# Kernel tuning notes

Measured on AMD Instinct MI355X. Metric: run time of the kernel, lower is better.

Reference implementation:

```python
import jax, jax.numpy as jnp
import numpy as np

B, T, D = 16, 2048, 512
DB, K, TOPK, WIN = 128, 7, 16, 64
GATE_CAP = 0.5
STRAND_CAP = 0.5
_PHI = 1.618033988749895
_PSI = -0.6180339887498949


def _ln(x, w, b):
    mu = jnp.mean(x, -1, keepdims=True)
    var = jnp.var(x, -1, keepdims=True)
    return (x - mu) * jax.lax.rsqrt(var + 1e-5) * w + b


def setup_inputs() -> dict:
    key = jax.random.key(0)
    ks = jax.random.split(key, 20)
    def nrm(i, shape, scale=1.0):
        return jax.random.normal(ks[i], shape, dtype=jnp.float32) * jnp.float32(scale)
    return {
        'X_write': nrm(0, (B, T, D)),
        'X_read': nrm(1, (B, T, D)),
        'slots': nrm(2, (B, K, DB)),
        'W0': nrm(3, (D, D), D ** -0.5),
        'ln_write_w': jnp.ones((D,), jnp.float32),
        'ln_write_b': jnp.zeros((D,), jnp.float32),
        'W_V': nrm(4, (D, DB), D ** -0.5),
        'W_K_slot': nrm(5, (DB, DB), DB ** -0.5),
        'slot_key_bias': nrm(6, (K, DB), 2.0),
        'W_gate_w': nrm(7, (2 * DB, DB), (2 * DB) ** -0.5),
        'W_gate_b': jnp.full((DB,), -2.0, jnp.float32),
        'ln_strand_w': jnp.ones((DB,), jnp.float32),
        'ln_strand_b': jnp.zeros((DB,), jnp.float32),
        'Ws_Q': nrm(8, (DB, DB), DB ** -0.5),
        'Ws_K': nrm(9, (DB, DB), DB ** -0.5),
        'Ws_V': nrm(10, (DB, DB), DB ** -0.5),
        'lambda_strand': nrm(11, (DB,), 0.5),
        'W_Q_read': nrm(12, (D, DB), D ** -0.5),
        'W_K_read': nrm(13, (DB, DB), DB ** -0.5),
        'W_V_read': nrm(14, (DB, D), DB ** -0.5),
        'render_coeffs': nrm(15, (K, 3, D), 0.2),
        'slot_temps': jnp.ones((K,), jnp.float32),
    }


def _forward(X_write, X_read, slots, W0, ln_write_w, ln_write_b, W_V, W_K_slot,
             slot_key_bias, W_gate_w, W_gate_b, ln_strand_w, ln_strand_b,
             Ws_Q, Ws_K, Ws_V, lambda_strand, W_Q_read, W_K_read, W_V_read,
             render_coeffs, slot_temps):
    scale = jnp.float32(DB ** -0.5)
    W0_sg = jax.lax.stop_gradient(W0)
    X_n = _ln(X_write, ln_write_w, ln_write_b)

    # ---- windowed salience + topk pair selection (no-grad in original) ----
    X_nsg = jax.lax.stop_gradient(X_n)
    X_W0 = X_nsg @ W0_sg.T                      # [B,T,D]
    NEG = jnp.float32(-1e30)
    sal = []
    for o in range(1, WIN + 1):                 # offset j = i - o, fixed small loop
        s = jnp.sum(X_nsg[:, o:, :] * X_W0[:, :-o, :], axis=-1)  # [B, T-o]
        sal.append(jnp.pad(s, ((0, 0), (o, 0)), constant_values=NEG))
    sal = jnp.stack(sal, axis=-1).reshape(B, T * WIN)
    _, flat_idx = jax.lax.top_k(sal, TOPK)      # [B, TOPK]
    i_idx = flat_idx // WIN
    j_idx = i_idx - (flat_idx % WIN + 1)

    # ---- gather pairs, salience-weighted relation vector ----
    x_newer = jnp.take_along_axis(X_n, i_idx[:, :, None], axis=1)   # [B,TOPK,D]
    x_older = jnp.take_along_axis(X_n, j_idx[:, :, None], axis=1)
    pair_sal = jnp.sum(x_newer * (x_older @ W0_sg.T), axis=-1)      # [B,TOPK]
    alpha = jax.nn.softmax(pair_sal, axis=-1)
    rel = (x_newer - x_older) @ W_V                                 # [B,TOPK,DB]
    R_t = jnp.einsum('bk,bkd->bd', alpha, rel)                      # [B,DB]

    # ---- gated slot write ----
    slot_keys = slots @ W_K_slot + slot_key_bias                    # [B,K,DB]
    compat = jnp.einsum('bkd,bd->bk', slot_keys, R_t) * scale * jax.nn.softplus(slot_temps)
    sw = jax.nn.softmax(compat, axis=-1)
    weighted_R = sw[:, :, None] * R_t[:, None, :]                   # [B,K,DB]
    g = jax.nn.sigmoid(jnp.concatenate([slots, weighted_R], -1) @ W_gate_w + W_gate_b)
    slots_upd = (1.0 - g) * slots + g * weighted_R

    # ---- K x K strand mixer ----
    Bn = _ln(slots_upd, ln_strand_w, ln_strand_b)
    sa = jax.nn.softmax(jnp.einsum('bqd,bkd->bqk', Bn @ Ws_Q, Bn @ Ws_K) * scale, axis=-1)
    ctx = sa @ (Bn @ Ws_V)
    slots_next = slots_upd + ctx * jnp.clip(jnp.tanh(lambda_strand), -STRAND_CAP, STRAND_CAP)

    # ---- aux losses ----
    L_persist = jnp.mean((slots_next - slots) ** 2)
    nrm = jnp.maximum(jnp.linalg.norm(slots_next, axis=-1, keepdims=True), 1e-12)
    Bnorm = slots_next / nrm
    cos = jnp.einsum('bkd,bjd->bkj', Bnorm, Bnorm)
    off = ~jnp.eye(K, dtype=bool)
    L_div = jnp.mean((cos ** 2)[:, off])

    # ---- directional gated read attention ----
    q_r = X_read @ W_Q_read                                         # [B,T,DB]
    k_r = slots_next @ W_K_read                                     # [B,K,DB]
    v_r = slots_next @ W_V_read                                     # [B,K,D]
    scores = jnp.einsum('btd,bkd->btk', q_r, k_r) * scale
    q_mean = jnp.mean(X_read, axis=1)                               # [B,D]
    w0q = q_mean @ W0_sg.T
    denom = jnp.float32(_PHI - _PSI)
    phi_q = (w0q - _PSI * q_mean) / denom
    psi_q = (_PHI * q_mean - w0q) / denom
    phi_mag = jnp.linalg.norm(phi_q, axis=-1, keepdims=True)
    psi_mag = jnp.linalg.norm(psi_q, axis=-1, keepdims=True)
    total = phi_mag + psi_mag + 1e-6
    basis = jnp.concatenate([jnp.ones_like(phi_mag), phi_mag / total, psi_mag / total], -1)  # [B,3]
    gate = jnp.clip(jnp.tanh(jnp.einsum('bi,kid->bkd', basis, render_coeffs)), -GATE_CAP, GATE_CAP)
    z = jnp.einsum('btk,bkd->btd', jax.nn.softmax(scores, axis=-1), v_r * gate)
    return z, slots_next, L_persist, L_div


def reference(X_write, X_read, slots, W0, ln_write_w, ln_write_b, W_V, W_K_slot,
              slot_key_bias, W_gate_w, W_gate_b, ln_strand_w, ln_strand_b,
              Ws_Q, Ws_K, Ws_V, lambda_strand, W_Q_read, W_K_read, W_V_read,
              render_coeffs, slot_temps):
    return _forward(X_write, X_read, slots, W0, ln_write_w, ln_write_b, W_V, W_K_slot,
                    slot_key_bias, W_gate_w, W_gate_b, ln_strand_w, ln_strand_b,
                    Ws_Q, Ws_K, Ws_V, lambda_strand, W_Q_read, W_K_read, W_V_read,
                    render_coeffs, slot_temps)
```

## Files before the change

### kernel.cpp

```cpp
#include <hip/hip_runtime.h>
#include <math.h>

#define B_ 16
#define T_ 2048
#define D_ 512
#define DB_ 128
#define K_ 7
#define TOPK_ 16
#define WIN_ 64

static constexpr float SCALE_ = 0.08838834764831845f;
static constexpr float PHI_ = 1.618033988749895f;
static constexpr float PSI_ = -0.6180339887498949f;
static constexpr float INV_DENOM_ = 0.4472135954999579f;
static constexpr float NEGV = -1e30f;
static constexpr float NEGINF = -3.402823466e38f;
#define IMAXI 0x7FFFFFFF

typedef __attribute__((ext_vector_type(8))) __bf16 bf16x8;
typedef __attribute__((ext_vector_type(8))) unsigned short u16x8;
typedef __attribute__((ext_vector_type(4))) float f32x4;

__device__ inline float softplusf(float x){
    return fmaxf(x, 0.f) + log1pf(expf(-fabsf(x)));
// ... 208 lines not shown
        rAh = *(const uint4*)(XhB + (size_t)(i0 + ar)*512 + kk + ac*8);
        rAl = *(const uint4*)(XlB + (size_t)(i0 + ar)*512 + kk + ac*8);
        #pragma unroll
        for (int cc = 0; cc < 2; cc++) {
            int c = 2*bhh + cc;
            if (jrow >= 0) {
                const float* src = CfB + (size_t)jrow*512 + kk + c*8;
                rB0[cc] = *(const float4*)src;
                rB1[cc] = *(const float4*)(src + 4);
            } else {
                rB0[cc] = make_float4(0.f,0.f,0.f,0.f);
                rB1[cc] = make_float4(0.f,0.f,0.f,0.f);
            }
        }
    };
    auto WRITE = [&](){
        *(uint4*)&sAh[ar*32 + aslot*8] = rAh;
        *(uint4*)&sAl[ar*32 + aslot*8] = rAl;
        #pragma unroll
        for (int cc = 0; cc < 2; cc++) {
            int c = 2*bhh + cc;
            int slot = (c + (brow >> 1)) & 3;
            uint4 hv, lv;
            float4 v0 = rB0[cc], v1 = rB1[cc];
            unsigned int h01 = pkbf(v0.x, v0.y), h23 = pkbf(v0.z, v0.w);
            unsigned int h45 = pkbf(v1.x, v1.y), h67 = pkbf(v1.z, v1.w);
            float r0 = v0.x - __uint_as_float(h01 << 16);
            float r1 = v0.y - __uint_as_float(h01 & 0xFFFF0000u);
            float r2 = v0.z - __uint_as_float(h23 << 16);
            float r3 = v0.w - __uint_as_float(h23 & 0xFFFF0000u);
            float r4 = v1.x - __uint_as_float(h45 << 16);
            float r5 = v1.y - __uint_as_float(h45 & 0xFFFF0000u);
            float r6 = v1.z - __uint_as_float(h67 << 16);
            float r7 = v1.w - __uint_as_float(h67 & 0xFFFF0000u);
            hv.x = h01; hv.y = h23; hv.z = h45; hv.w = h67;
            lv.x = pkbf(r0, r1); lv.y = pkbf(r2, r3); lv.z = pkbf(r4, r5); lv.w = pkbf(r6, r7);
            *(uint4*)&sBh[brow*32 + slot*8] = hv;
            *(uint4*)&sBl[brow*32 + slot*8] = lv;
        }
    };

    LOAD(0);
    for (int t = 0; t < 16; t++) {
        WRITE();
        __syncthreads();
        int kkn = (t+1)*32;
        bf16x8 ahf[4], alf[4], bhf[2], blf[2];
        #pragma unroll
        for (int m = 0; m < 4; m++) {
            int r = (m*16 + fr)*32 + kc2;
            ahf[m] = ld_bf8(&sAh[r]);
            alf[m] = ld_bf8(&sAl[r]);
        }
        #pragma unroll
        for (int n = 0; n < 2; n++) {
            int r = (wcw*32 + n*16 + fr)*32 + kc2;
            bhf[n] = ld_bf8(&sBh[r]);
            blf[n] = ld_bf8(&sBl[r]);
        }
        if (t < 15) LOAD(kkn);
        #pragma unroll
        for (int m = 0; m < 4; m++)
            #pragma unroll
            for (int n = 0; n < 2; n++) {
                acc[m][n] = __builtin_amdgcn_mfma_f32_16x16x32_bf16(ahf[m], bhf[n], acc[m][n], 0, 0, 0);
                acc[m][n] = __builtin_amdgcn_mfma_f32_16x16x32_bf16(ahf[m], blf[n], acc[m][n], 0, 0, 0);
                acc[m][n] = __builtin_amdgcn_mfma_f32_16x16x32_bf16(alf[m], bhf[n], acc[m][n], 0, 0, 0);
            }
        __syncthreads();
    }

    float* salB = sal + (size_t)b*T_*WIN_;
    #pragma unroll
    for (int m = 0; m < 4; m++) {
        #pragma unroll
        for (int n = 0; n < 2; n++) {
            int jl = wcw*32 + n*16 + fr;
            #pragma unroll
            for (int r = 0; r < 4; r++) {
                int il = m*16 + (lane >> 4)*4 + r;
                int o = il - jl + 64;
                if (o >= 1 && o <= 64) {
                    int jg = i0 - 64 + jl;
                    salB[(size_t)(i0 + il)*WIN_ + (o - 1)] = (jg >= 0) ? acc[m][n][r] : NEGV;
                }
            }
        }
    }
}

__global__ __launch_bounds__(256) void topk_stage1(const float* __restrict__ sal,
                                                   float* __restrict__ cv, int* __restrict__ ci,
                                                   const float* __restrict__ qpart,
                                                   const float* __restrict__ W0,
                                                   float* __restrict__ w0p)
{
    int b = blockIdx.x, tid = threadIdx.x;
    if (blockIdx.y >= 64) {
        int c = blockIdx.y - 64;
        __shared__ float qm[D_];
        for (int p = tid; p < D_; p += 256) {
            float s = 0.f;
            for (int cc = 0; cc < 32; cc++) s += qpart[((size_t)b*32 + cc)*D_ + p];
            qm[p] = s * (1.f/2048.f);
        }
        __syncthreads();
        int w = tid >> 6, lane = tid & 63;
        float ph = 0.f, ps = 0.f;
        for (int r = 0; r < 16; r++) {
            int d = c*64 + w*16 + r;
            const float* wr = W0 + (size_t)d*D_;
            float s = 0.f;
            #pragma unroll
            for (int q = 0; q < 8; q++) s += qm[lane + q*64] * wr[lane + q*64];
            #pragma unroll
            for (int off = 32; off; off >>= 1) s += __shfl_xor(s, off);
            float phi = (s - PSI_*qm[d]) * INV_DENOM_;
            float psi = (PHI_*qm[d] - s) * INV_DENOM_;
            ph += phi*phi; ps += psi*psi;
        }
        __shared__ float shp[4], shs[4];
        if (lane == 0) { shp[w] = ph; shs[w] = ps; }
        __syncthreads();
        if (tid == 0) {
            w0p[((size_t)b*8 + c)*2 + 0] = shp[0]+shp[1]+shp[2]+shp[3];
            w0p[((size_t)b*8 + c)*2 + 1] = shs[0]+shs[1]+shs[2]+shs[3];
        }
        return;
    }
    int c = blockIdx.y;
    const float* s = sal + (size_t)b*(T_*WIN_) + (size_t)c*2048;
    int base = c*2048;
    int lane = tid & 63, wvi = tid >> 6;
    float v0=NEGINF,v1=NEGINF,v2=NEGINF,v3=NEGINF,v4=NEGINF,v5=NEGINF,v6=NEGINF,v7=NEGINF;
    int   i0=IMAXI, i1=IMAXI, i2=IMAXI, i3=IMAXI, i4=IMAXI, i5=IMAXI, i6=IMAXI, i7=IMAXI;
    #pragma unroll
    for (int r = 0; r < 8; r++) {
        int p = tid + r*256;
        float v = s[p];
        int idx = base + p;
        if (v > v7 || (v == v7 && idx < i7)) {
            bool b6 = (v > v6) || (v == v6 && idx < i6);
            bool b5 = (v > v5) || (v == v5 && idx < i5);
            bool b4 = (v > v4) || (v == v4 && idx < i4);
            bool b3 = (v > v3) || (v == v3 && idx < i3);
            bool b2 = (v > v2) || (v == v2 && idx < i2);
            bool b1 = (v > v1) || (v == v1 && idx < i1);
            bool b0 = (v > v0) || (v == v0 && idx < i0);
            float n7 = b6 ? v6 : v;             int m7 = b6 ? i6 : idx;
            float n6 = b6 ? (b5 ? v5 : v) : v6; int m6 = b6 ? (b5 ? i5 : idx) : i6;
            float n5 = b5 ? (b4 ? v4 : v) : v5; int m5 = b5 ? (b4 ? i4 : idx) : i5;
            float n4 = b4 ? (b3 ? v3 : v) : v4; int m4 = b4 ? (b3 ? i3 : idx) : i4;
            float n3 = b3 ? (b2 ? v2 : v) : v3; int m3 = b3 ? (b2 ? i2 : idx) : i3;
            float n2 = b2 ? (b1 ? v1 : v) : v2; int m2 = b2 ? (b1 ? i1 : idx) : i2;
            float n1 = b1 ? (b0 ? v0 : v) : v1; int m1 = b1 ? (b0 ? i0 : idx) : i1;
            float n0 = b0 ? v : v0;             int m0 = b0 ? idx : i0;
            v7=n7;i7=m7; v6=n6;i6=m6; v5=n5;i5=m5; v4=n4;i4=m4;
            v3=n3;i3=m3; v2=n2;i2=m2; v1=n1;i1=m1; v0=n0;i0=m0;
        }
    }
    float* cvo = cv + (((size_t)b*64 + c)*64) + wvi*16;
    int*   cio = ci + (((size_t)b*64 + c)*64) + wvi*16;
    for (int r = 0; r < 16; r++) {
        float bv = v0; int bi = i0;
        float wv_ = bv; int wi = bi;
        #pragma unroll
        for (int off = 1; off < 64; off <<= 1) {
            float vx = __shfl_xor(wv_, off);
            int   ix = __shfl_xor(wi, off);
            if (vx > wv_ || (vx == wv_ && ix < wi)) { wv_ = vx; wi = ix; }
        }
        if (bv == wv_ && bi == wi) {
            v0=v1;i0=i1; v1=v2;i1=i2; v2=v3;i2=i3; v3=v4;i3=i4;
            v4=v5;i4=i5; v5=v6;i5=i6; v6=v7;i6=i7; v7=NEGINF;i7=IMAXI;
        }
        if (lane == 0) { cvo[r] = wv_; cio[r] = wi; }
    }
}

__global__ __launch_bounds__(512) void slot_head(
    const unsigned short* __restrict__ Xh, const unsigned short* __restrict__ Xl,
    const float* __restrict__ cv, const int* __restrict__ ci,
    float* __restrict__ yws)
{
    int b = blockIdx.x, tid = threadIdx.x;
    int lane = tid & 63, wvi = tid >> 6;
    __shared__ float scv[128]; __shared__ int sci[128];
    __shared__ float tvv[16]; __shared__ int tii[16];
    __shared__ float alpha[16]; __shared__ int tis[16], tjs[16];

    const float* cvb = cv + (size_t)b*4096;
    const int*   cib = ci + (size_t)b*4096;
    float v0=NEGINF,v1=NEGINF,v2=NEGINF,v3=NEGINF,v4=NEGINF,v5=NEGINF,v6=NEGINF,v7=NEGINF;
    int   i0=IMAXI, i1=IMAXI, i2=IMAXI, i3=IMAXI, i4=IMAXI, i5=IMAXI, i6=IMAXI, i7=IMAXI;
    #pragma unroll
    for (int r = 0; r < 8; r++) {
        int p = tid + r*512;
        float v = cvb[p];
        int idx = cib[p];
        if (v > v7 || (v == v7 && idx < i7)) {
            bool b6 = (v > v6) || (v == v6 && idx < i6);
            bool b5 = (v > v5) || (v == v5 && idx < i5);
            bool b4 = (v > v4) || (v == v4 && idx < i4);
            bool b3 = (v > v3) || (v == v3 && idx < i3);
            bool b2 = (v > v2) || (v == v2 && idx < i2);
            bool b1 = (v > v1) || (v == v1 && idx < i1);
            bool b0 = (v > v0) || (v == v0 && idx < i0);
            float n7 = b6 ? v6 : v;             int m7 = b6 ? i6 : idx;
            float n6 = b6 ? (b5 ? v5 : v) : v6; int m6 = b6 ? (b5 ? i5 : idx) : i6;
            float n5 = b5 ? (b4 ? v4 : v) : v5; int m5 = b5 ? (b4 ? i4 : idx) : i5;
            float n4 = b4 ? (b3 ? v3 : v) : v4; int m4 = b4 ? (b3 ? i3 : idx) : i4;
            float n3 = b3 ? (b2 ? v2 : v) : v3; int m3 = b3 ? (b2 ? i2 : idx) : i3;
            float n2 = b2 ? (b1 ? v1 : v) : v2; int m2 = b2 ? (b1 ? i1 : idx) : i2;
            float n1 = b1 ? (b0 ? v0 : v) : v1; int m1 = b1 ? (b0 ? i0 : idx) : i1;
            float n0 = b0 ? v : v0;             int m0 = b0 ? idx : i0;
            v7=n7;i7=m7; v6=n6;i6=m6; v5=n5;i5=m5; v4=n4;i4=m4;
            v3=n3;i3=m3; v2=n2;i2=m2; v1=n1;i1=m1; v0=n0;i0=m0;
        }
    }
    for (int r = 0; r < 16; r++) {
        float bv = v0; int bi = i0;
        float wv_ = bv; int wi = bi;
        #pragma unroll
        for (int off = 1; off < 64; off <<= 1) {
            float vx = __shfl_xor(wv_, off);
            int   ix = __shfl_xor(wi, off);
            if (vx > wv_ || (vx == wv_ && ix < wi)) { wv_ = vx; wi = ix; }
        }
        if (bv == wv_ && bi == wi) {
            v0=v1;i0=i1; v1=v2;i1=i2; v2=v3;i2=i3; v3=v4;i3=i4;
            v4=v5;i4=i5; v5=v6;i5=i6; v6=v7;i6=i7; v7=NEGINF;i7=IMAXI;
        }
        if (lane == 0) { scv[wvi*16 + r] = wv_; sci[wvi*16 + r] = wi; }
    }
    __syncthreads();
    if (wvi == 0) {
        float a0 = scv[lane], a1 = scv[lane + 64];
        int   e0 = sci[lane], e1 = sci[lane + 64];
        bool sw = (a1 > a0) || (a1 == a0 && e1 < e0);
        float u0 = sw ? a1 : a0; int j0 = sw ? e1 : e0;
        float u1 = sw ? a0 : a1; int j1 = sw ? e0 : e1;
        for (int r = 0; r < 16; r++) {
            float bv = u0; int bi = j0;
            float wv_ = bv; int wi = bi;
            #pragma unroll
            for (int off = 1; off < 64; off <<= 1) {
                float vx = __shfl_xor(wv_, off);
                int   ix = __shfl_xor(wi, off);
                if (vx > wv_ || (vx == wv_ && ix < wi)) { wv_ = vx; wi = ix; }
            }
            if (bv == wv_ && bi == wi) { u0 = u1; j0 = j1; u1 = NEGINF; j1 = IMAXI; }
            if (lane == 0) { tvv[r] = wv_; tii[r] = wi; }
        }
    }
    __syncthreads();
    if (tid < 16) {
        float v = tvv[tid];
        int flat = tii[tid];
        tis[tid] = flat >> 6;
        tjs[tid] = (flat >> 6) - ((flat & 63) + 1);
        float m = v;
        #pragma unroll
        for (int off = 8; off; off >>= 1) m = fmaxf(m, __shfl_xor(m, off, 16));
        float e = expf(v - m);
        float s = e;
        #pragma unroll
        for (int off = 8; off; off >>= 1) s += __shfl_xor(s, off, 16);
        alpha[tid] = e / s;
    }
    __syncthreads();
    {
        float acc = 0.f;
        #pragma unroll
        for (int k = 0; k < 16; k++) {
            int i = tis[k], j = tjs[k];
            float xi = bf2f(Xh[((size_t)b*T_ + i)*D_ + tid]) + bf2f(Xl[((size_t)b*T_ + i)*D_ + tid]);
            float xj = bf2f(Xh[((size_t)b*T_ + j)*D_ + tid]) + bf2f(Xl[((size_t)b*T_ + j)*D_ + tid]);
            acc += alpha[k] * (xi - xj);
        }
        yws[(size_t)b*D_ + tid] = acc;
    }
}

__global__ __launch_bounds__(256) void slot_rt(const float* __restrict__ yws,
                                               const float* __restrict__ W_V,
                                               float* __restrict__ rtp)
{
    int b = blockIdx.x, c = blockIdx.y, tid = threadIdx.x;
    __shared__ float ysl[64];
    __shared__ float hsum[2][DB_];
    if (tid < 64) ysl[tid] = yws[(size_t)b*D_ + c*64 + tid];
    __syncthreads();
    int d = tid & 127, h = tid >> 7;
    float acc = 0.f;
    int e0 = h*32;
    #pragma unroll 8
    for (int e = e0; e < e0 + 32; e++)
        acc += ysl[e] * W_V[(size_t)(c*64 + e)*DB_ + d];
    hsum[h][d] = acc;
    __syncthreads();
    if (tid < DB_) rtp[((size_t)b*8 + c)*DB_ + tid] = hsum[0][tid] + hsum[1][tid];
}

__global__ __launch_bounds__(1024) void slot_main(
    const float* __restrict__ slots_in, const float* __restrict__ rtp,
    const float* __restrict__ W_K_slot, const float* __restrict__ skb,
    const float* __restrict__ Wg, const float* __restrict__ Wgb,
    const float* __restrict__ lnw, const float* __restrict__ lnb,
    const float* __restrict__ WsQ, const float* __restrict__ WsK, const float* __restrict__ WsV,
    const float* __restrict__ lambda_, const float* __restrict__ temps,
    float* __restrict__ snws, float* __restrict__ out_slots,
    float* __restrict__ lpP, float* __restrict__ lpD)
{
    int b = blockIdx.x, tid = threadIdx.x;
    int lane = tid & 63, wvi = tid >> 6;
    __shared__ __align__(16) float wbuf[2*8192];
    __shared__ float Rt[DB_];
    __shared__ float sl[K_][DB_];
    __shared__ float upd[K_][DB_];
    __shared__ float Bn[K_][DB_];
    __shared__ float qq[K_][DB_], kk2[K_][DB_], vv[K_][DB_];
    __shared__ float snsh[K_][DB_];
    __shared__ float pf[1024];
    __shared__ float swv[K_], compat[K_], mu7[K_], rs7[K_], nr7[K_], ldv[K_];
    __shared__ float sa[K_][K_];

    auto ISSUE = [&](const float* src, int buf){
        const float* g = src + (wvi*2)*256 + lane*4;
        float* l = wbuf + buf*8192 + (wvi*2)*256;
        gload16(g, l);
        gload16(g + 256, l + 256);
    };

    int kk_ = tid >> 7, dd_ = tid & 127;
    bool act = tid < K_*DB_;

    ISSUE(W_K_slot, 0);
    for (int p = tid; p < K_*DB_; p += 1024) sl[p>>7][p&127] = slots_in[(size_t)b*K_*DB_ + p];
    if (tid < DB_) {
        float a = 0.f;
        #pragma unroll
        for (int c = 0; c < 8; c++) a += rtp[((size_t)b*8 + c)*DB_ + tid];
        Rt[tid] = a;
    }
    __syncthreads();
    ISSUE(W_K_slot + 8192, 1);
    float kacc = 0.f;
    if (act) {
        #pragma unroll 8
        for (int e = 0; e < 64; e++) kacc += sl[kk_][e] * wbuf[e*DB_ + dd_];
    }
    __syncthreads();
    ISSUE(Wg, 0);
    if (act) {
        #pragma unroll 8
        for (int e = 0; e < 64; e++) kacc += sl[kk_][64+e] * wbuf[8192 + e*DB_ + dd_];
        qq[kk_][dd_] = (kacc + skb[kk_*DB_ + dd_]) * Rt[dd_];
    }
    __syncthreads();
    if (wvi < K_) {
        float acc = qq[wvi][lane] + qq[wvi][lane + 64];
        #pragma unroll
        for (int off = 32; off; off >>= 1) acc += __shfl_xor(acc, off);
        if (lane == 0) compat[wvi] = acc * SCALE_ * softplusf(temps[wvi]);
    }
    __syncthreads();
    if (tid == 0) {
        float m = compat[0];
        for (int k = 1; k < K_; k++) m = fmaxf(m, compat[k]);
        float ssum = 0.f;
        for (int k = 0; k < K_; k++) { float e = expf(compat[k]-m); swv[k] = e; ssum += e; }
        for (int k = 0; k < K_; k++) swv[k] /= ssum;
    }
    __syncthreads();
    ISSUE(Wg + 8192, 1);
    float gacc = 0.f;
    if (act) {
        #pragma unroll 8
        for (int e = 0; e < 64; e++) gacc += sl[kk_][e] * wbuf[e*DB_ + dd_];
    }
    __syncthreads();
    ISSUE(Wg + 16384, 0);
    if (act) {
        #pragma unroll 8
        for (int e = 0; e < 64; e++) gacc += sl[kk_][64+e] * wbuf[8192 + e*DB_ + dd_];
    }
    __syncthreads();
    ISSUE(Wg + 24576, 1);
    float g2acc = 0.f;
    if (act) {
        #pragma unroll 8
        for (int e = 0; e < 64; e++) g2acc += Rt[e] * wbuf[e*DB_ + dd_];
    }
    __syncthreads();
    ISSUE(WsQ, 0);
    if (act) {
        #pragma unroll 8
        for (int e = 0; e < 64; e++) g2acc += Rt[64+e] * wbuf[8192 + e*DB_ + dd_];
        float pre = gacc + swv[kk_]*g2acc + Wgb[dd_];
        float g = 1.f / (1.f + expf(-pre));
        upd[kk_][dd_] = (1.f - g) * sl[kk_][dd_] + g * (swv[kk_] * Rt[dd_]);
    }
    __syncthreads();
    if (wvi < K_) {
        float a0 = upd[wvi][lane], a1 = upd[wvi][lane + 64];
        float s = a0 + a1, ss = a0*a0 + a1*a1;
        #pragma unroll
        for (int off = 32; off; off >>= 1) { s += __shfl_xor(s, off); ss += __shfl_xor(ss, off); }
        if (lane == 0) {
            float mu = s / (float)DB_;
            mu7[wvi] = mu;
            rs7[wvi] = rsqrtf(ss/(float)DB_ - mu*mu + 1e-5f);
        }
    }
    __syncthreads();
    if (act) Bn[kk_][dd_] = (upd[kk_][dd_] - mu7[kk_]) * rs7[kk_] * lnw[dd_] + lnb[dd_];
    __syncthreads();
    ISSUE(WsQ + 8192, 1);
    float qacc = 0.f;
    if (act) {
        #pragma unroll 8
        for (int e = 0; e < 64; e++) qacc += Bn[kk_][e] * wbuf[e*DB_ + dd_];
    }
    __syncthreads();
    ISSUE(WsK, 0);
    if (act) {
        #pragma unroll 8
        for (int e = 0; e < 64; e++) qacc += Bn[kk_][64+e] * wbuf[8192 + e*DB_ + dd_];
        qq[kk_][dd_] = qacc;
    }
    __syncthreads();
    ISSUE(WsK + 8192, 1);
    float kacc2 = 0.f;
    if (act) {
        #pragma unroll 8
        for (int e = 0; e < 64; e++) kacc2 += Bn[kk_][e] * wbuf[e*DB_ + dd_];
    }
    __syncthreads();
    ISSUE(WsV, 0);
    if (act) {
        #pragma unroll 8
        for (int e = 0; e < 64; e++) kacc2 += Bn[kk_][64+e] * wbuf[8192 + e*DB_ + dd_];
        kk2[kk_][dd_] = kacc2;
    }
    __syncthreads();
    ISSUE(WsV + 8192, 1);
    float vacc = 0.f;
    if (act) {
        #pragma unroll 8
        for (int e = 0; e < 64; e++) vacc += Bn[kk_][e] * wbuf[e*DB_ + dd_];
    }
    __syncthreads();
    if (act) {
        #pragma unroll 8
        for (int e = 0; e < 64; e++) vacc += Bn[kk_][64+e] * wbuf[8192 + e*DB_ + dd_];
        vv[kk_][dd_] = vacc;
    }
    __syncthreads();

    if (wvi < K_) {
        int j = lane >> 3, s = lane & 7;
        float acc = 0.f;
        if (j < K_) {
            int e0 = s * 16;
            for (int e = e0; e < e0 + 16; e++) acc += qq[wvi][e] * kk2[j][e];
        }
        #pragma unroll
        for (int off = 4; off; off >>= 1) acc += __shfl_xor(acc, off, 8);
        if (s == 0 && j < K_) sa[wvi][j] = acc * SCALE_;
    }
    __syncthreads();
    if (tid < K_) {
        float m = sa[tid][0];
        for (int j = 1; j < K_; j++) m = fmaxf(m, sa[tid][j]);
        float ssum = 0.f;
        for (int j = 0; j < K_; j++) { float e = expf(sa[tid][j]-m); sa[tid][j] = e; ssum += e; }
        for (int j = 0; j < K_; j++) sa[tid][j] /= ssum;
    }
    __syncthreads();
    if (act) {
        float lam = tanhf(lambda_[dd_]);
        lam = fminf(fmaxf(lam, -0.5f), 0.5f);
        float c = 0.f;
        #pragma unroll
        for (int j = 0; j < K_; j++) c += sa[kk_][j] * vv[j][dd_];
        float sn = upd[kk_][dd_] + c * lam;
        snsh[kk_][dd_] = sn;
        snws[((size_t)b*K_ + kk_)*DB_ + dd_] = sn;
        out_slots[((size_t)b*K_ + kk_)*DB_ + dd_] = sn;
    }
    __syncthreads();
    {
        float dsq = 0.f;
        if (act) { float dd2 = snsh[kk_][dd_] - sl[kk_][dd_]; dsq = dd2*dd2; }
        pf[tid] = dsq;
        if (wvi < K_) {
            float a0 = snsh[wvi][lane], a1 = snsh[wvi][lane + 64];
            float ss = a0*a0 + a1*a1;
            #pragma unroll
            for (int off = 32; off; off >>= 1) ss += __shfl_xor(ss, off);
            if (lane == 0) nr7[wvi] = fmaxf(sqrtf(ss), 1e-12f);
        }
        __syncthreads();
        if (wvi == 0) {
            float s = 0.f;
            #pragma unroll
            for (int q = 0; q < 16; q++) s += pf[lane + q*64];
            #pragma unroll
            for (int off = 32; off; off >>= 1) s += __shfl_xor(s, off);
            if (lane == 0) lpP[b] = s;
        }
        if (wvi >= 1 && wvi <= K_) {
            int q = wvi - 1;
            float accq = 0.f;
            for (int j = 0; j < K_; j++) {
                if (j == q) continue;
                float dt = snsh[q][lane]*snsh[j][lane] + snsh[q][lane+64]*snsh[j][lane+64];
                #pragma unroll
                for (int off = 32; off; off >>= 1) dt += __shfl_xor(dt, off);
                float cs = dt / (nr7[q] * nr7[j]);
                accq += cs*cs;
            }
            if (lane == 0) ldv[q] = accq;
        }
        __syncthreads();
        if (tid == 0) {
            float s = 0.f;
            for (int q = 0; q < K_; q++) s += ldv[q];
            lpD[b] = s;
        }
    }
}

__global__ __launch_bounds__(256) void kqvg_kernel(
    const float* __restrict__ sn, const float* __restrict__ WKr,
    const float* __restrict__ WQr, const float* __restrict__ WVr,
    const float* __restrict__ rc, const float* __restrict__ w0p,
    const float* __restrict__ lpP, const float* __restrict__ lpD,
    float* __restrict__ kq, float* __restrict__ vg, float* __restrict__ loss_out)
{
    int b = blockIdx.x, k = blockIdx.y, tid = threadIdx.x;
    if (b == 0 && k == 0 && tid == 0) {
        float s = 0.f, s2 = 0.f;
        for (int bb = 0; bb < B_; bb++) { s += lpP[bb]; s2 += lpD[bb]; }
        loss_out[0] = s / (float)(B_*K_*DB_);
        loss_out[1] = s2 / (float)(B_*(K_*K_-K_));
    }
    float P = 0.f, Q = 0.f;
    #pragma unroll
    for (int c = 0; c < 8; c++) {
        P += w0p[((size_t)b*8 + c)*2 + 0];
        Q += w0p[((size_t)b*8 + c)*2 + 1];
    }
    float pm = sqrtf(P), qm2 = sqrtf(Q);
    float tot = pm + qm2 + 1e-6f;
    float b1 = pm / tot, b2 = qm2 / tot;

    __shared__ float sl[DB_], kr[DB_];
    if (tid < DB_) sl[tid] = sn[((size_t)b*K_ + k)*DB_ + tid];
    __syncthreads();
    if (tid < DB_) {
        float a = 0.f;
        for (int e = 0; e < DB_; e++) a += sl[e] * WKr[(size_t)e*DB_ + tid];
        kr[tid] = a;
    }
    __syncthreads();
    #pragma unroll
    for (int rep = 0; rep < 2; rep++) {
        int e = tid + rep*256;
        float a = 0.f;
        const float* wq = WQr + (size_t)e*DB_;
        for (int d = 0; d < DB_; d++) a += kr[d] * wq[d];
        kq[((size_t)b*K_ + k)*D_ + e] = a;
    }
    #pragma unroll
    for (int rep = 0; rep < 2; rep++) {
        int dd = tid + rep*256;
        float a = 0.f;
        for (int e = 0; e < DB_; e++) a += sl[e] * WVr[(size_t)e*D_ + dd];
        float gpre = rc[((size_t)k*3 + 0)*D_ + dd] + b1*rc[((size_t)k*3 + 1)*D_ + dd] + b2*rc[((size_t)k*3 + 2)*D_ + dd];
        float g = tanhf(gpre);
        g = fminf(fmaxf(g, -0.5f), 0.5f);
        vg[((size_t)b*K_ + k)*D_ + dd] = a * g;
    }
}

__global__ __launch_bounds__(256) void z_kernel(const float* __restrict__ Xr,
                                                const float* __restrict__ kq,
                                                const float* __restrict__ vg,
                                                float* __restrict__ z)
{
    int b = blockIdx.x;
    int t0 = blockIdx.y * 64;
    __shared__ float kqs[K_][D_];
    __shared__ float vgs[K_][D_];
    int tid = threadIdx.x;
    for (int p = tid; p < K_*D_; p += 256) {
        kqs[p>>9][p&511] = kq[(size_t)b*K_*D_ + p];
        vgs[p>>9][p&511] = vg[(size_t)b*K_*D_ + p];
    }
    __syncthreads();
    int lane = tid & 63, w = tid >> 6;
    for (int it = 0; it < 16; it++) {
        int t = t0 + w*16 + it;
        const float* x = Xr + ((size_t)b*T_ + t)*D_;
        float xr[8];
        float s[K_] = {0,0,0,0,0,0,0};
        #pragma unroll
        for (int r = 0; r < 8; r++) {
            int e = lane + r*64;
            xr[r] = x[e];
            #pragma unroll
            for (int k = 0; k < K_; k++) s[k] += xr[r] * kqs[k][e];
        }
        #pragma unroll
        for (int k = 0; k < K_; k++)
            for (int off = 32; off; off >>= 1) s[k] += __shfl_xor(s[k], off);
        float sc[K_];
        float m = NEGINF;
        #pragma unroll
        for (int k = 0; k < K_; k++) { sc[k] = s[k] * SCALE_; m = fmaxf(m, sc[k]); }
        float p[K_], ssum = 0.f;
        #pragma unroll
        for (int k = 0; k < K_; k++) { p[k] = expf(sc[k] - m); ssum += p[k]; }
        float inv = 1.f / ssum;
        float* zp = z + ((size_t)b*T_ + t)*D_;
        #pragma unroll
        for (int r = 0; r < 8; r++) {
            int e = lane + r*64;
            float a = 0.f;
            #pragma unroll
            for (int k = 0; k < K_; k++) a += p[k] * vgs[k][e];
            zp[e] = a * inv;
        }
    }
}

extern "C" void kernel_launch(void* const* d_in, const int* in_sizes, int n_in,
                              void* d_out, int out_size, void* d_ws, size_t ws_size,
                              hipStream_t stream)
{
    const float* X_write = (const float*)d_in[0];
    const float* X_read  = (const float*)d_in[1];
    const float* slots   = (const float*)d_in[2];
    const float* W0      = (const float*)d_in[3];
    const float* lnw_w   = (const float*)d_in[4];
    const float* lnw_b   = (const float*)d_in[5];
    const float* W_V     = (const float*)d_in[6];
    const float* W_K_slot= (const float*)d_in[7];
    const float* skb     = (const float*)d_in[8];
    const float* Wg      = (const float*)d_in[9];
    const float* Wgb     = (const float*)d_in[10];
    const float* lns_w   = (const float*)d_in[11];
    const float* lns_b   = (const float*)d_in[12];
    const float* WsQ     = (const float*)d_in[13];
    const float* WsK     = (const float*)d_in[14];
    const float* WsV     = (const float*)d_in[15];
    const float* lambda_ = (const float*)d_in[16];
    const float* WQr     = (const float*)d_in[17];
    const float* WKr     = (const float*)d_in[18];
    const float* WVr     = (const float*)d_in[19];
    const float* rc      = (const float*)d_in[20];
    const float* temps   = (const float*)d_in[21];

    const size_t NXD = (size_t)B_*T_*D_;
    unsigned short* Xh  = (unsigned short*)d_ws;
    unsigned short* Xl  = Xh + NXD;
    float* Cf           = (float*)(Xl + NXD);
    unsigned short* W0h = (unsigned short*)(Cf + NXD);
    unsigned short* W0l = W0h + (size_t)D_*D_;
    float* fscr  = (float*)(W0l + (size_t)D_*D_);
    float* qpart = fscr;
    float* w0p   = qpart + (size_t)B_*32*D_;
    float* snws  = w0p + 256;
    float* kq    = snws + (size_t)B_*K_*DB_;
    float* vg    = kq + (size_t)B_*K_*D_;
    float* cv    = vg + (size_t)B_*K_*D_;
    int*   ci    = (int*)(cv + (size_t)B_*64*64);
    float* lpP   = (float*)(ci + (size_t)B_*64*64);
    float* lpD   = lpP + 16;
    float* yws   = lpD + 16;
    float* rtp   = yws + (size_t)B_*D_;

    float* z_out     = (float*)d_out;
    float* slots_out = z_out + NXD;
    float* loss_out  = slots_out + (size_t)B_*K_*DB_;
    float* sal       = z_out;

    prep_kernel<<<dim3(4096 + 256 + 512), dim3(256), 0, stream>>>(
        X_write, lnw_w, lnw_b, Xh, Xl, W0, W0h, W0l, X_read, qpart);
    gemm_xw0_mfma<<<dim3(B_*T_/128, D_/128), dim3(256), 0, stream>>>(Xh, Xl, W0h, W0l, Cf);
    sal_mfma<<<dim3(B_, T_/64), dim3(256), 0, stream>>>(Xh, Xl, Cf, sal);
    topk_stage1<<<dim3(B_, 72), dim3(256), 0, stream>>>(sal, cv, ci, qpart, W0, w0p);
    slot_head<<<dim3(B_), dim3(512), 0, stream>>>(Xh, Xl, cv, ci, yws);
    slot_rt<<<dim3(B_, 8), dim3(256), 0, stream>>>(yws, W_V, rtp);
    slot_main<<<dim3(B_), dim3(1024), 0, stream>>>(slots, rtp,
        W_K_slot, skb, Wg, Wgb, lns_w, lns_b, WsQ, WsK, WsV, lambda_, temps,
        snws, slots_out, lpP, lpD);
    kqvg_kernel<<<dim3(B_, K_), dim3(256), 0, stream>>>(snws, WKr, WQr, WVr, rc, w0p,
        lpP, lpD, kq, vg, loss_out);
    z_kernel<<<dim3(B_, T_/64), dim3(256), 0, stream>>>(X_read, kq, vg, z_out);
}
```

Measured before the change: 265.5 us.

## Split serial slot_main kernel into four parallel kernels across more blocks

The single 16-block slot update kernel, which streamed every weight matrix serially through shared memory, becomes four kernels. The first computes the slot key and gate projections across 256 blocks, the second does the softmax, gate and layernorm per batch, the third runs the Q/K/V projections across 192 blocks, and the fourth does the strand attention and losses. The aim is to use many more compute units for the small matmuls instead of 16 long serial blocks. In exchange it adds three extra launches and round trips of intermediates through global memory.

```diff
diff --git a/kernel.cpp b/kernel.cpp
--- a/kernel.cpp
+++ b/kernel.cpp
@@ -534,67 +534,102 @@
     if (tid < DB_) rtp[((size_t)b*8 + c)*DB_ + tid] = hsum[0][tid] + hsum[1][tid];
 }
 
-__global__ __launch_bounds__(1024) void slot_main(
+__global__ __launch_bounds__(256) void slot_w1(
     const float* __restrict__ slots_in, const float* __restrict__ rtp,
     const float* __restrict__ W_K_slot, const float* __restrict__ skb,
-    const float* __restrict__ Wg, const float* __restrict__ Wgb,
-    const float* __restrict__ lnw, const float* __restrict__ lnb,
-    const float* __restrict__ WsQ, const float* __restrict__ WsK, const float* __restrict__ WsV,
-    const float* __restrict__ lambda_, const float* __restrict__ temps,
-    float* __restrict__ snws, float* __restrict__ out_slots,
-    float* __restrict__ lpP, float* __restrict__ lpD)
-{
-    int b = blockIdx.x, tid = threadIdx.x;
-    int lane = tid & 63, wvi = tid >> 6;
-    __shared__ __align__(16) float wbuf[2*8192];
+    const float* __restrict__ Wg,
+    float* __restrict__ skvw, float* __restrict__ gp1w, float* __restrict__ gp2w)
+{
+    int b = blockIdx.x, dc = blockIdx.y * 8, tid = threadIdx.x;
+    __shared__ float sl[K_][DB_];
     __shared__ float Rt[DB_];
-    __shared__ float sl[K_][DB_];
-    __shared__ float upd[K_][DB_];
-    __shared__ float Bn[K_][DB_];
-    __shared__ float qq[K_][DB_], kk2[K_][DB_], vv[K_][DB_];
-    __shared__ float snsh[K_][DB_];
-    __shared__ float pf[1024];
-    __shared__ float swv[K_], compat[K_], mu7[K_], rs7[K_], nr7[K_], ldv[K_];
-    __shared__ float sa[K_][K_];
-
-    auto ISSUE = [&](const float* src, int buf){
-        const float* g = src + (wvi*2)*256 + lane*4;
-        float* l = wbuf + buf*8192 + (wvi*2)*256;
-        gload16(g, l);
-        gload16(g + 256, l + 256);
-    };
-
-    int kk_ = tid >> 7, dd_ = tid & 127;
-    bool act = tid < K_*DB_;
-
-    ISSUE(W_K_slot, 0);
-    for (int p = tid; p < K_*DB_; p += 1024) sl[p>>7][p&127] = slots_in[(size_t)b*K_*DB_ + p];
+    __shared__ float w0s[DB_][9], w1s[DB_][9], w2s[DB_][9];
+    __shared__ float parA[224], parB[224], parC[32];
+    for (int p = tid; p < K_*DB_; p += 256) sl[p>>7][p&127] = slots_in[(size_t)b*K_*DB_ + p];
     if (tid < DB_) {
         float a = 0.f;
         #pragma unroll
         for (int c = 0; c < 8; c++) a += rtp[((size_t)b*8 + c)*DB_ + tid];
         Rt[tid] = a;
     }
-    __syncthreads();
-    ISSUE(W_K_slot + 8192, 1);
-    float kacc = 0.f;
-    if (act) {
+    if (tid < 128) {
+        float4 a0 = *(const float4*)&W_K_slot[(size_t)tid*DB_ + dc];
+        float4 a1 = *(const float4*)&W_K_slot[(size_t)tid*DB_ + dc + 4];
+        w0s[tid][0]=a0.x; w0s[tid][1]=a0.y; w0s[tid][2]=a0.z; w0s[tid][3]=a0.w;
+        w0s[tid][4]=a1.x; w0s[tid][5]=a1.y; w0s[tid][6]=a1.z; w0s[tid][7]=a1.w;
+        float4 b0 = *(const float4*)&Wg[(size_t)tid*DB_ + dc];
+        float4 b1 = *(const float4*)&Wg[(size_t)tid*DB_ + dc + 4];
+        w1s[tid][0]=b0.x; w1s[tid][1]=b0.y; w1s[tid][2]=b0.z; w1s[tid][3]=b0.w;
+        w1s[tid][4]=b1.x; w1s[tid][5]=b1.y; w1s[tid][6]=b1.z; w1s[tid][7]=b1.w;
+        float4 c0 = *(const float4*)&Wg[(size_t)(DB_ + tid)*DB_ + dc];
+        float4 c1 = *(const float4*)&Wg[(size_t)(DB_ + tid)*DB_ + dc + 4];
+        w2s[tid][0]=c0.x; w2s[tid][1]=c0.y; w2s[tid][2]=c0.z; w2s[tid][3]=c0.w;
+        w2s[tid][4]=c1.x; w2s[tid][5]=c1.y; w2s[tid][6]=c1.z; w2s[tid][7]=c1.w;
+    }
+    __syncthreads();
+    if (tid < 224) {
+        int k = tid >> 5, rem = tid & 31, dloc = rem >> 2, e4 = rem & 3;
+        float a0 = 0.f, a1 = 0.f;
+        int e0 = e4*32;
         #pragma unroll 8
-        for (int e = 0; e < 64; e++) kacc += sl[kk_][e] * wbuf[e*DB_ + dd_];
-    }
-    __syncthreads();
-    ISSUE(Wg, 0);
-    if (act) {
+        for (int e = e0; e < e0+32; e++) {
+            float sv = sl[k][e];
+            a0 += sv * w0s[e][dloc];
+            a1 += sv * w1s[e][dloc];
+        }
+        parA[tid] = a0; parB[tid] = a1;
+    } else {
+        int t2 = tid - 224;
+        int dloc = t2 >> 2, e4 = t2 & 3;
+        float a = 0.f;
+        int e0 = e4*32;
         #pragma unroll 8
-        for (int e = 0; e < 64; e++) kacc += sl[kk_][64+e] * wbuf[8192 + e*DB_ + dd_];
-        qq[kk_][dd_] = (kacc + skb[kk_*DB_ + dd_]) * Rt[dd_];
-    }
-    __syncthreads();
-    if (wvi < K_) {
-        float acc = qq[wvi][lane] + qq[wvi][lane + 64];
-        #pragma unroll
-        for (int off = 32; off; off >>= 1) acc += __shfl_xor(acc, off);
-        if (lane == 0) compat[wvi] = acc * SCALE_ * softplusf(temps[wvi]);
+        for (int e = e0; e < e0+32; e++) a += Rt[e] * w2s[e][dloc];
+        parC[t2] = a;
+    }
+    __syncthreads();
+    if (tid < 56) {
+        int k = tid >> 3, dloc = tid & 7;
+        int base = k*32 + dloc*4;
+        float a0 = parA[base] + parA[base+1] + parA[base+2] + parA[base+3];
+        float a1 = parB[base] + parB[base+1] + parB[base+2] + parB[base+3];
+        int d = dc + dloc;
+        skvw[((size_t)b*K_ + k)*DB_ + d] = (a0 + skb[k*DB_ + d]) * Rt[d];
+        gp1w[((size_t)b*K_ + k)*DB_ + d] = a1;
+    } else if (tid < 64) {
+        int dloc = tid - 56;
+        int base = dloc*4;
+        gp2w[(size_t)b*DB_ + dc + dloc] = parC[base] + parC[base+1] + parC[base+2] + parC[base+3];
+    }
+}
+
+__global__ __launch_bounds__(256) void slot_w2(
+    const float* __restrict__ slots_in, const float* __restrict__ rtp,
+    const float* __restrict__ skvw, const float* __restrict__ gp1w,
+    const float* __restrict__ gp2w, const float* __restrict__ Wgb,
+    const float* __restrict__ lnw, const float* __restrict__ lnb,
+    const float* __restrict__ temps,
+    float* __restrict__ updw, float* __restrict__ bnw)
+{
+    int b = blockIdx.x, tid = threadIdx.x;
+    __shared__ float sl[K_][DB_], Rt[DB_], upd[K_][DB_];
+    __shared__ float compat[K_], swv[K_], mu7[K_], rs7[K_];
+    for (int p = tid; p < K_*DB_; p += 256) sl[p>>7][p&127] = slots_in[(size_t)b*K_*DB_ + p];
+    if (tid < DB_) {
+        float a = 0.f;
+        #pragma unroll
+        for (int c = 0; c < 8; c++) a += rtp[((size_t)b*8 + c)*DB_ + tid];
+        Rt[tid] = a;
+    }
+    __syncthreads();
+    int g = tid >> 5, l32 = tid & 31;
+    if (g < K_) {
+        float a = 0.f;
+        #pragma unroll
+        for (int r = 0; r < 4; r++) a += skvw[((size_t)b*K_ + g)*DB_ + l32 + r*32];
+        #pragma unroll
+        for (int off = 16; off; off >>= 1) a += __shfl_xor(a, off);
+        if (l32 == 0) compat[g] = a * SCALE_ * softplusf(temps[g]);
     }
     __syncthreads();
     if (tid == 0) {
@@ -605,91 +640,87 @@
         for (int k = 0; k < K_; k++) swv[k] /= ssum;
     }
     __syncthreads();
-    ISSUE(Wg + 8192, 1);
-    float gacc = 0.f;
-    if (act) {
+    #pragma unroll
+    for (int r = 0; r < 4; r++) {
+        int idx = tid + r*256;
+        if (idx < K_*DB_) {
+            int k = idx >> 7, d = idx & 127;
+            float pre = gp1w[(size_t)b*K_*DB_ + idx] + swv[k]*gp2w[(size_t)b*DB_ + d] + Wgb[d];
+            float gg = 1.f / (1.f + expf(-pre));
+            float u = (1.f - gg)*sl[k][d] + gg*(swv[k]*Rt[d]);
+            upd[k][d] = u;
+            updw[(size_t)b*K_*DB_ + idx] = u;
+        }
+    }
+    __syncthreads();
+    if (g < K_) {
+        float s = 0.f, ss = 0.f;
+        #pragma unroll
+        for (int r = 0; r < 4; r++) { float v = upd[g][l32 + r*32]; s += v; ss += v*v; }
+        #pragma unroll
+        for (int off = 16; off; off >>= 1) { s += __shfl_xor(s, off); ss += __shfl_xor(ss, off); }
+        if (l32 == 0) {
+            float mu = s / (float)DB_;
+            mu7[g] = mu;
+            rs7[g] = rsqrtf(ss/(float)DB_ - mu*mu + 1e-5f);
+        }
+    }
+    __syncthreads();
+    #pragma unroll
+    for (int r = 0; r < 4; r++) {
+        int idx = tid + r*256;
+        if (idx < K_*DB_) {
+            int k = idx >> 7, d = idx & 127;
+            bnw[(size_t)b*K_*DB_ + idx] = (upd[k][d] - mu7[k])*rs7[k]*lnw[d] + lnb[d];
+        }
+    }
+}
+
+__global__ __launch_bounds__(256) void slot_qkv(const float* __restrict__ bnw,
+    const float* __restrict__ WsQ, const float* __restrict__ WsK, const float* __restrict__ WsV,
+    float* __restrict__ qkvw)
+{
+    int b = blockIdx.x, m = blockIdx.y >> 2, dc = (blockIdx.y & 3) * 32, tid = threadIdx.x;
+    const float* W = (m == 0) ? WsQ : (m == 1) ? WsK : WsV;
+    __shared__ float Bn[K_][DB_];
+    __shared__ float ws[DB_][32];
+    for (int p = tid; p < K_*DB_; p += 256) Bn[p>>7][p&127] = bnw[(size_t)b*K_*DB_ + p];
+    #pragma unroll
+    for (int i = 0; i < 16; i++) {
+        int idx = tid + i*256;
+        int row = idx >> 5, col = idx & 31;
+        ws[row][col] = W[(size_t)row*DB_ + dc + col];
+    }
+    __syncthreads();
+    if (tid < 224) {
+        int k = tid >> 5, dloc = tid & 31;
+        float a = 0.f;
         #pragma unroll 8
-        for (int e = 0; e < 64; e++) gacc += sl[kk_][e] * wbuf[e*DB_ + dd_];
-    }
-    __syncthreads();
-    ISSUE(Wg + 16384, 0);
-    if (act) {
-        #pragma unroll 8
-        for (int e = 0; e < 64; e++) gacc += sl[kk_][64+e] * wbuf[8192 + e*DB_ + dd_];
-    }
-    __syncthreads();
-    ISSUE(Wg + 24576, 1);
-    float g2acc = 0.f;
-    if (act) {
-        #pragma unroll 8
-        for (int e = 0; e < 64; e++) g2acc += Rt[e] * wbuf[e*DB_ + dd_];
-    }
-    __syncthreads();
-    ISSUE(WsQ, 0);
-    if (act) {
-        #pragma unroll 8
-        for (int e = 0; e < 64; e++) g2acc += Rt[64+e] * wbuf[8192 + e*DB_ + dd_];
-        float pre = gacc + swv[kk_]*g2acc + Wgb[dd_];
-        float g = 1.f / (1.f + expf(-pre));
-        upd[kk_][dd_] = (1.f - g) * sl[kk_][dd_] + g * (swv[kk_] * Rt[dd_]);
-    }
-    __syncthreads();
-    if (wvi < K_) {
-        float a0 = upd[wvi][lane], a1 = upd[wvi][lane + 64];
-        float s = a0 + a1, ss = a0*a0 + a1*a1;
-        #pragma unroll
-        for (int off = 32; off; off >>= 1) { s += __shfl_xor(s, off); ss += __shfl_xor(ss, off); }
-        if (lane == 0) {
-            float mu = s / (float)DB_;
-            mu7[wvi] = mu;
-            rs7[wvi] = rsqrtf(ss/(float)DB_ - mu*mu + 1e-5f);
-        }
-    }
-    __syncthreads();
-    if (act) Bn[kk_][dd_] = (upd[kk_][dd_] - mu7[kk_]) * rs7[kk_] * lnw[dd_] + lnb[dd_];
-    __syncthreads();
-    ISSUE(WsQ + 8192, 1);
-    float qacc = 0.f;
-    if (act) {
-        #pragma unroll 8
-        for (int e = 0; e < 64; e++) qacc += Bn[kk_][e] * wbuf[e*DB_ + dd_];
-    }
-    __syncthreads();
-    ISSUE(WsK, 0);
-    if (act) {
-        #pragma unroll 8
-        for (int e = 0; e < 64; e++) qacc += Bn[kk_][64+e] * wbuf[8192 + e*DB_ + dd_];
-        qq[kk_][dd_] = qacc;
-    }
-    __syncthreads();
-    ISSUE(WsK + 8192, 1);
-    float kacc2 = 0.f;
-    if (act) {
-        #pragma unroll 8
-        for (int e = 0; e < 64; e++) kacc2 += Bn[kk_][e] * wbuf[e*DB_ + dd_];
-    }
-    __syncthreads();
-    ISSUE(WsV, 0);
-    if (act) {
-        #pragma unroll 8
-        for (int e = 0; e < 64; e++) kacc2 += Bn[kk_][64+e] * wbuf[8192 + e*DB_ + dd_];
-        kk2[kk_][dd_] = kacc2;
-    }
-    __syncthreads();
-    ISSUE(WsV + 8192, 1);
-    float vacc = 0.f;
-    if (act) {
-        #pragma unroll 8
-        for (int e = 0; e < 64; e++) vacc += Bn[kk_][e] * wbuf[e*DB_ + dd_];
-    }
-    __syncthreads();
-    if (act) {
-        #pragma unroll 8
-        for (int e = 0; e < 64; e++) vacc += Bn[kk_][64+e] * wbuf[8192 + e*DB_ + dd_];
-        vv[kk_][dd_] = vacc;
-    }
-    __syncthreads();
-
+        for (int e = 0; e < DB_; e++) a += Bn[k][e] * ws[e][dloc];
+        qkvw[(((size_t)m*B_ + b)*K_ + k)*DB_ + dc + dloc] = a;
+    }
+}
+
+__global__ __launch_bounds__(512) void slot_fin(
+    const float* __restrict__ slots_in, const float* __restrict__ updw,
+    const float* __restrict__ qkvw, const float* __restrict__ lambda_,
+    float* __restrict__ snws, float* __restrict__ out_slots,
+    float* __restrict__ lpP, float* __restrict__ lpD)
+{
+    int b = blockIdx.x, tid = threadIdx.x;
+    int lane = tid & 63, wvi = tid >> 6;
+    __shared__ float upd[K_][DB_], qq[K_][DB_], kk2[K_][DB_], vv[K_][DB_], sl[K_][DB_], snsh[K_][DB_];
+    __shared__ float sa[K_][K_], nr7[K_], ldv[K_];
+    __shared__ float pf[512];
+    for (int p = tid; p < K_*DB_; p += 512) {
+        int k = p >> 7, d = p & 127;
+        upd[k][d] = updw[(size_t)b*K_*DB_ + p];
+        qq[k][d]  = qkvw[(((size_t)0*B_ + b)*K_*DB_) + p];
+        kk2[k][d] = qkvw[(((size_t)1*B_ + b)*K_*DB_) + p];
+        vv[k][d]  = qkvw[(((size_t)2*B_ + b)*K_*DB_) + p];
+        sl[k][d]  = slots_in[(size_t)b*K_*DB_ + p];
+    }
+    __syncthreads();
     if (wvi < K_) {
         int j = lane >> 3, s = lane & 7;
         float acc = 0.f;
@@ -710,57 +741,61 @@
         for (int j = 0; j < K_; j++) sa[tid][j] /= ssum;
     }
     __syncthreads();
-    if (act) {
-        float lam = tanhf(lambda_[dd_]);
-        lam = fminf(fmaxf(lam, -0.5f), 0.5f);
-        float c = 0.f;
-        #pragma unroll
-        for (int j = 0; j < K_; j++) c += sa[kk_][j] * vv[j][dd_];
-        float sn = upd[kk_][dd_] + c * lam;
-        snsh[kk_][dd_] = sn;
-        snws[((size_t)b*K_ + kk_)*DB_ + dd_] = sn;
-        out_slots[((size_t)b*K_ + kk_)*DB_ + dd_] = sn;
-    }
-    __syncthreads();
-    {
-        float dsq = 0.f;
-        if (act) { float dd2 = snsh[kk_][dd_] - sl[kk_][dd_]; dsq = dd2*dd2; }
-        pf[tid] = dsq;
-        if (wvi < K_) {
-            float a0 = snsh[wvi][lane], a1 = snsh[wvi][lane + 64];
-            float ss = a0*a0 + a1*a1;
-            #pragma unroll
-            for (int off = 32; off; off >>= 1) ss += __shfl_xor(ss, off);
-            if (lane == 0) nr7[wvi] = fmaxf(sqrtf(ss), 1e-12f);
-        }
-        __syncthreads();
-        if (wvi == 0) {
-            float s = 0.f;
-            #pragma unroll
-            for (int q = 0; q < 16; q++) s += pf[lane + q*64];
-            #pragma unroll
-            for (int off = 32; off; off >>= 1) s += __shfl_xor(s, off);
-            if (lane == 0) lpP[b] = s;
-        }
-        if (wvi >= 1 && wvi <= K_) {
-            int q = wvi - 1;
-            float accq = 0.f;
-            for (int j = 0; j < K_; j++) {
-                if (j == q) continue;
-                float dt = snsh[q][lane]*snsh[j][lane] + snsh[q][lane+64]*snsh[j][lane+64];
-                #pragma unroll
-                for (int off = 32; off; off >>= 1) dt += __shfl_xor(dt, off);
-                float cs = dt / (nr7[q] * nr7[j]);
-                accq += cs*cs;
-            }
-            if (lane == 0) ldv[q] = accq;
-        }
-        __syncthreads();
-        if (tid == 0) {
-            float s = 0.f;
-            for (int q = 0; q < K_; q++) s += ldv[q];
-            lpD[b] = s;
-        }
+    float dsq = 0.f;
+    #pragma unroll
+    for (int r = 0; r < 2; r++) {
+        int idx = tid + r*512;
+        if (idx < K_*DB_) {
+            int k = idx >> 7, d = idx & 127;
+            float lam = tanhf(lambda_[d]);
+            lam = fminf(fmaxf(lam, -0.5f), 0.5f);
+            float c = 0.f;
+            #pragma unroll
+            for (int j = 0; j < K_; j++) c += sa[k][j] * vv[j][d];
+            float sn = upd[k][d] + c * lam;
+            snsh[k][d] = sn;
+            snws[(size_t)b*K_*DB_ + idx] = sn;
+            out_slots[(size_t)b*K_*DB_ + idx] = sn;
+            float ddf = sn - sl[k][d];
+            dsq += ddf*ddf;
+        }
+    }
+    __syncthreads();
+    pf[tid] = dsq;
+    if (wvi < K_) {
+        float a0 = snsh[wvi][lane], a1 = snsh[wvi][lane + 64];
+        float ss = a0*a0 + a1*a1;
+        #pragma unroll
+        for (int off = 32; off; off >>= 1) ss += __shfl_xor(ss, off);
+        if (lane == 0) nr7[wvi] = fmaxf(sqrtf(ss), 1e-12f);
+    }
+    __syncthreads();
+    if (wvi == 0) {
+        float s = 0.f;
+        #pragma unroll
+        for (int q = 0; q < 8; q++) s += pf[lane + q*64];
+        #pragma unroll
+        for (int off = 32; off; off >>= 1) s += __shfl_xor(s, off);
+        if (lane == 0) lpP[b] = s;
+    }
+    if (wvi >= 1 && wvi <= K_) {
+        int q = wvi - 1;
+        float accq = 0.f;
+        for (int j = 0; j < K_; j++) {
+            if (j == q) continue;
+            float dt = snsh[q][lane]*snsh[j][lane] + snsh[q][lane+64]*snsh[j][lane+64];
+            #pragma unroll
+            for (int off = 32; off; off >>= 1) dt += __shfl_xor(dt, off);
+            float cs = dt / (nr7[q] * nr7[j]);
+            accq += cs*cs;
+        }
+        if (lane == 0) ldv[q] = accq;
+    }
+    __syncthreads();
+    if (tid == 0) {
+        float s = 0.f;
+        for (int q = 0; q < K_; q++) s += ldv[q];
+        lpD[b] = s;
     }
 }
 
@@ -908,11 +943,17 @@
     float* kq    = snws + (size_t)B_*K_*DB_;
     float* vg    = kq + (size_t)B_*K_*D_;
     float* cv    = vg + (size_t)B_*K_*D_;
-    int*   ci    = (int*)(cv + (size_t)B_*64*64);
-    float* lpP   = (float*)(ci + (size_t)B_*64*64);
+    int*   ci    = (int*)(cv + (size_t)B_*4096);
+    float* lpP   = (float*)(ci + (size_t)B_*4096);
     float* lpD   = lpP + 16;
     float* yws   = lpD + 16;
     float* rtp   = yws + (size_t)B_*D_;
+    float* skvw  = rtp + (size_t)B_*8*DB_;
+    float* gp1w  = skvw + (size_t)B_*K_*DB_;
+    float* gp2w  = gp1w + (size_t)B_*K_*DB_;
+    float* updw  = gp2w + (size_t)B_*DB_;
+    float* bnw   = updw + (size_t)B_*K_*DB_;
+    float* qkvw  = bnw + (size_t)B_*K_*DB_;
 
     float* z_out     = (float*)d_out;
     float* slots_out = z_out + NXD;
@@ -926,8 +967,12 @@
     topk_stage1<<<dim3(B_, 72), dim3(256), 0, stream>>>(sal, cv, ci, qpart, W0, w0p);
     slot_head<<<dim3(B_), dim3(512), 0, stream>>>(Xh, Xl, cv, ci, yws);
     slot_rt<<<dim3(B_, 8), dim3(256), 0, stream>>>(yws, W_V, rtp);
-    slot_main<<<dim3(B_), dim3(1024), 0, stream>>>(slots, rtp,
-        W_K_slot, skb, Wg, Wgb, lns_w, lns_b, WsQ, WsK, WsV, lambda_, temps,
+    slot_w1<<<dim3(B_, 16), dim3(256), 0, stream>>>(slots, rtp, W_K_slot, skb, Wg,
+        skvw, gp1w, gp2w);
+    slot_w2<<<dim3(B_), dim3(256), 0, stream>>>(slots, rtp, skvw, gp1w, gp2w, Wgb,
+        lns_w, lns_b, temps, updw, bnw);
+    slot_qkv<<<dim3(B_, 12), dim3(256), 0, stream>>>(bnw, WsQ, WsK, WsV, qkvw);
+    slot_fin<<<dim3(B_), dim3(512), 0, stream>>>(slots, updw, qkvw, lambda_,
         snws, slots_out, lpP, lpD);
     kqvg_kernel<<<dim3(B_, K_), dim3(256), 0, stream>>>(snws, WKr, WQr, WVr, rc, w0p,
         lpP, lpD, kq, vg, loss_out);
```

After: 255.9 us, median of 2. 1.04x faster.
